# Performance work log

Measured on AMD Instinct MI355X. Metric: run time of the kernel, lower is better.

The kernel has to match this reference:

```python
import jax, jax.numpy as jnp
import numpy as np
import math

HEADS = 8
DIM_HEAD = 64
DIM = HEADS * DIM_HEAD  # 512; to_v is Identity so dim must equal heads*dim_head
SCALE = DIM_HEAD ** -0.5


def get_slopes(n):
    def pow2(n):
        start = 2 ** (-2 ** (-(math.log2(n) - 3)))
        return [start * start ** i for i in range(n)]
    if math.log2(n).is_integer():
        return pow2(n)
    c = 2 ** math.floor(math.log2(n))
    return pow2(c) + get_slopes(2 * c)[0::2][: n - c]

SLOPES = jnp.asarray(np.array(get_slopes(HEADS), dtype=np.float32))


def setup_inputs() -> dict:
    key = jax.random.key(0)
    k1, k2, k3, k4 = jax.random.split(key, 4)
    b, n = 4, 2048
    x = jax.random.normal(k1, (b, n, DIM), dtype=jnp.float32)
    # positions: e.g. observation timestamps (days); uniform floats scaled to [0, 365)
    positions = jax.random.uniform(k2, (b, n), dtype=jnp.float32) * 365.0
    Wq = jax.random.normal(k3, (DIM, DIM), dtype=jnp.float32) * (DIM ** -0.5)
    Wk = jax.random.normal(k4, (DIM, DIM), dtype=jnp.float32) * (DIM ** -0.5)
    return {"x": x, "positions": positions, "Wq": Wq, "Wk": Wk}


def reference(x, positions, Wq, Wk):
    b, n, _ = x.shape
    # q, k projections (no bias); v = x (Identity)
    q = (x @ Wq.T).reshape(b, n, HEADS, DIM_HEAD).transpose(0, 2, 1, 3)  # b h n d
    k = (x @ Wk.T).reshape(b, n, HEADS, DIM_HEAD).transpose(0, 2, 1, 3)
    v = x.reshape(b, n, HEADS, DIM_HEAD).transpose(0, 2, 1, 3)
    dots = jnp.einsum('bhid,bhjd->bhij', q, k) * SCALE  # b h n n
    # relative_positions[b,i,j] = -|positions[b,j] - positions[b,i]|
    rel = -jnp.abs(positions[:, None, :] - positions[:, :, None])  # b n n
    alibi = SLOPES[None, :, None, None] * rel[:, None, :, :]  # b h n n
    attn = jax.nn.softmax(dots + alibi, axis=-1)
    out = jnp.einsum('bhij,bhjd->bhid', attn, v)  # b h n d
    return out.transpose(0, 2, 1, 3).reshape(b, n, DIM)
```

## Files before the change

### kernel.cpp

```cpp
#include <hip/hip_runtime.h>
#include <hip/hip_bf16.h>

typedef __bf16 bf16x8 __attribute__((ext_vector_type(8)));
typedef float f32x4 __attribute__((ext_vector_type(4)));
typedef float f32x16 __attribute__((ext_vector_type(16)));

__device__ inline unsigned short f2bf(float f) {
    __hip_bfloat16 h = __float2bfloat16(f);
    return __builtin_bit_cast(unsigned short, h);
}
__device__ inline unsigned pk2bf(float a, float b) {
    return (unsigned)f2bf(a) | ((unsigned)f2bf(b) << 16);
}
__device__ inline float exp2_fast(float x) {
    float r;
    asm("v_exp_f32 %0, %1" : "=v"(r) : "v"(x));
    return r;
}

#define QSCALE 0.1803368801111244f

__global__ __launch_bounds__(256) void xpose_v(const float* __restrict__ x,
                                               unsigned short* __restrict__ Vt) {
    const int tid = threadIdx.x;
    const int lane = tid & 63, w = tid >> 6;
    const int b = blockIdx.z, h = blockIdx.y;
    const int n = blockIdx.x * 256 + w * 64 + lane;
    const int np = (n & ~15) | (n & 3) | ((n & 4) << 1) | ((n & 8) >> 1);
    const size_t xrow = ((size_t)b * 2048 + n) * 512 + h * 64;
    const size_t vbase = ((size_t)(b * 8 + h) * 64) * 2048 + np;
#pragma unroll
    for (int d0 = 0; d0 < 64; d0 += 4) {
        float4 v = *reinterpret_cast<const float4*>(&x[xrow + d0]);
        Vt[vbase + (size_t)(d0 + 0) * 2048] = f2bf(v.x);
        Vt[vbase + (size_t)(d0 + 1) * 2048] = f2bf(v.y);
        Vt[vbase + (size_t)(d0 + 2) * 2048] = f2bf(v.z);
        Vt[vbase + (size_t)(d0 + 3) * 2048] = f2bf(v.w);
    }
}

__global__ __launch_bounds__(256) void gemm_qk(const float* __restrict__ x,
                                               const float* __restrict__ Wq,
                                               const float* __restrict__ Wk,
                                               unsigned short* __restrict__ Qb,
                                               unsigned short* __restrict__ Kb) {
    __shared__ __align__(16) unsigned short sA[128 * 40];
    __shared__ __align__(16) unsigned short sB[128 * 40];
    const int tid  = threadIdx.x;
    const int lane = tid & 63;
    const int wave = tid >> 6;
    const int wr = wave >> 1, wc = wave & 1;
    const int bm = blockIdx.x * 128;
    const int by = blockIdx.y;
    const float* __restrict__ Bsrc = (by < 4) ? Wq : Wk;
    unsigned short* __restrict__ C = (by < 4) ? Qb : Kb;
    const int bn = (by & 3) * 128;
    const float scale = (by < 4) ? QSCALE : 1.0f;
    const int tr = tid >> 1, th = (tid & 1) * 16;
    const int rl = lane & 15;
    const int kq = (lane >> 4) * 8;

    f32x4 acc[4][4];
#pragma unroll
    for (int m = 0; m < 4; ++m)
#pragma unroll
        for (int n = 0; n < 4; ++n) acc[m][n] = (f32x4){0.f, 0.f, 0.f, 0.f};

    for (int k0 = 0; k0 < 512; k0 += 32) {
        const float* ap = &x[(size_t)(bm + tr) * 512 + k0 + th];
        const float* bp = &Bsrc[(size_t)(bn + tr) * 512 + k0 + th];
        float4 a0 = *reinterpret_cast<const float4*>(ap);
        float4 a1 = *reinterpret_cast<const float4*>(ap + 4);
        float4 a2 = *reinterpret_cast<const float4*>(ap + 8);
        float4 a3 = *reinterpret_cast<const float4*>(ap + 12);
        float4 b0 = *reinterpret_cast<const float4*>(bp);
        float4 b1 = *reinterpret_cast<const float4*>(bp + 4);
        float4 b2 = *reinterpret_cast<const float4*>(bp + 8);
        float4 b3 = *reinterpret_cast<const float4*>(bp + 12);
        uint4 pa0 = {pk2bf(a0.x, a0.y), pk2bf(a0.z, a0.w), pk2bf(a1.x, a1.y), pk2bf(a1.z, a1.w)};
        uint4 pa1 = {pk2bf(a2.x, a2.y), pk2bf(a2.z, a2.w), pk2bf(a3.x, a3.y), pk2bf(a3.z, a3.w)};
        uint4 pb0 = {pk2bf(b0.x, b0.y), pk2bf(b0.z, b0.w), pk2bf(b1.x, b1.y), pk2bf(b1.z, b1.w)};
        uint4 pb1 = {pk2bf(b2.x, b2.y), pk2bf(b2.z, b2.w), pk2bf(b3.x, b3.y), pk2bf(b3.z, b3.w)};
        __syncthreads();
        *reinterpret_cast<uint4*>(&sA[tr * 40 + th])     = pa0;
        *reinterpret_cast<uint4*>(&sA[tr * 40 + th + 8]) = pa1;
        *reinterpret_cast<uint4*>(&sB[tr * 40 + th])     = pb0;
        *reinterpret_cast<uint4*>(&sB[tr * 40 + th + 8]) = pb1;
        __syncthreads();

        bf16x8 af[4], bfv[4];
#pragma unroll
        for (int m = 0; m < 4; ++m)
            af[m] = __builtin_bit_cast(bf16x8,
                *reinterpret_cast<const uint4*>(&sA[(wr * 64 + m * 16 + rl) * 40 + kq]));
#pragma unroll
        for (int n = 0; n < 4; ++n)
            bfv[n] = __builtin_bit_cast(bf16x8,
                *reinterpret_cast<const uint4*>(&sB[(wc * 64 + n * 16 + rl) * 40 + kq]));
#pragma unroll
        for (int m = 0; m < 4; ++m)
#pragma unroll
            for (int n = 0; n < 4; ++n)
                acc[m][n] = __builtin_amdgcn_mfma_f32_16x16x32_bf16(af[m], bfv[n], acc[m][n], 0, 0, 0);
    }

    const int rq = (lane >> 4) * 4;
#pragma unroll
    for (int m = 0; m < 4; ++m) {
        int r = bm + wr * 64 + m * 16 + rq;
#pragma unroll
        for (int n = 0; n < 4; ++n) {
            int c = bn + wc * 64 + n * 16 + rl;
#pragma unroll
            for (int reg = 0; reg < 4; ++reg)
                C[(size_t)(r + reg) * 512 + c] = f2bf(acc[m][n][reg] * scale);
        }
    }
}

__global__ __launch_bounds__(512, 4) void attn_fwd(const unsigned short* __restrict__ Q,
                                                   const unsigned short* __restrict__ Kb,
                                                   const unsigned short* __restrict__ Vt,
                                                   const float* __restrict__ pos,
                                                   float* __restrict__ Out) {
    __shared__ __align__(16) unsigned char smem[34304];
    char* k0b = (char*)smem;
    char* v0b = (char*)smem + 8192;
    char* k1b = (char*)smem + 16384;
    char* v1b = (char*)smem + 24576;
    float* p0b = (float*)(smem + 32768);
    float* p1b = (float*)(smem + 33024);
    float* sMl = (float*)(smem + 33280);

    const int tid  = threadIdx.x;
    const int lane = tid & 63;
    const int w    = tid >> 6;
    const int l31  = lane & 31;
    const int hi   = lane >> 5;
    const int qh   = w & 3;
    const int jp   = w >> 2;
    const int b = blockIdx.z, h = blockIdx.y;
    const int q0 = blockIdx.x * 128 + qh * 32;
    const size_t rowbase = (size_t)b * 2048;
    const int hc = h * 64;
    const int bh = b * 8 + h;
    const float slopeL = ldexpf(1.4426950408889634f, -(h + 1));

    bf16x8 qf0, qf1, qf2, qf3;
    {
        const unsigned short* qp = &Q[(rowbase + q0 + l31) * 512 + hc + hi * 8];
        qf0 = __builtin_bit_cast(bf16x8, *reinterpret_cast<const uint4*>(qp));
        qf1 = __builtin_bit_cast(bf16x8, *reinterpret_cast<const uint4*>(qp + 16));
        qf2 = __builtin_bit_cast(bf16x8, *reinterpret_cast<const uint4*>(qp + 32));
        qf3 = __builtin_bit_cast(bf16x8, *reinterpret_cast<const uint4*>(qp + 48));
    }
    const float ui = slopeL * pos[rowbase + q0 + l31];

    float lloc = 0.f;
    f32x16 o0, o1;
#pragma unroll
    for (int r = 0; r < 16; ++r) { o0[r] = 0.f; o1[r] = 0.f; }

    const int sr  = tid >> 3;
    const int sce = (tid & 7) * 8;
    const int wbyte = sr * 128 + (((tid & 7) * 16) ^ ((sr & 7) << 4));
    const int kswz = (l31 & 7) << 4;

    uint4 ck, cv;
    float cpj = 0.f;

    auto stage = [&](int j0v) {
        ck = *reinterpret_cast<const uint4*>(&Kb[(rowbase + j0v + sr) * 512 + hc + sce]);
        cv = *reinterpret_cast<const uint4*>(&Vt[((size_t)bh * 64 + sr) * 2048 + j0v + sce]);
        if (tid < 64) cpj = pos[rowbase + j0v + tid];
    };
    auto writeb = [&](char* KB, char* VB, float* PB) {
        *reinterpret_cast<uint4*>(KB + wbyte) = ck;
        *reinterpret_cast<uint4*>(VB + wbyte) = cv;
        if (tid < 64) PB[tid] = slopeL * cpj;
    };
    auto compute = [&](const char* KB, const char* VB, const float* PB) {
        const char* kr = KB + (32 * jp + l31) * 128;
        f32x16 s;
#pragma unroll
        for (int r = 0; r < 16; ++r) s[r] = 0.f;
        __builtin_amdgcn_s_setprio(1);
#pragma unroll
        for (int ks = 0; ks < 4; ++ks) {
            bf16x8 kf = __builtin_bit_cast(bf16x8,
                *reinterpret_cast<const uint4*>(kr + ((ks * 32 + hi * 16) ^ kswz)));
            bf16x8 qq = (ks == 0) ? qf0 : (ks == 1) ? qf1 : (ks == 2) ? qf2 : qf3;
            s = __builtin_amdgcn_mfma_f32_32x32x16_bf16(kf, qq, s, 0, 0, 0);
        }
        __builtin_amdgcn_s_setprio(0);

        float ls = 0.f;
#pragma unroll
        for (int t = 0; t < 4; ++t) {
            f32x4 u = *reinterpret_cast<const f32x4*>(&PB[32 * jp + 8 * t + 4 * hi]);
#pragma unroll
            for (int r = 0; r < 4; ++r) {
                float p = exp2_fast(s[4 * t + r] - fabsf(u[r] - ui));
                s[4 * t + r] = p;
                ls += p;
            }
        }
        lloc += ls;

        bf16x8 pf0 = __builtin_bit_cast(bf16x8, (uint4){
            pk2bf(s[0], s[1]),  pk2bf(s[2], s[3]),   pk2bf(s[4], s[5]),   pk2bf(s[6], s[7])});
        bf16x8 pf1 = __builtin_bit_cast(bf16x8, (uint4){
            pk2bf(s[8], s[9]),  pk2bf(s[10], s[11]), pk2bf(s[12], s[13]), pk2bf(s[14], s[15])});

        const char* vr0 = VB + l31 * 128;
        const char* vr1 = VB + (32 + l31) * 128;
        __builtin_amdgcn_s_setprio(1);
#pragma unroll
        for (int ks = 0; ks < 2; ++ks) {
            const int cb = 64 * jp + ks * 32 + hi * 16;
            bf16x8 v0 = __builtin_bit_cast(bf16x8,
                *reinterpret_cast<const uint4*>(vr0 + (cb ^ kswz)));
            bf16x8 v1 = __builtin_bit_cast(bf16x8,
                *reinterpret_cast<const uint4*>(vr1 + (cb ^ kswz)));
            bf16x8 pf = ks ? pf1 : pf0;
            o0 = __builtin_amdgcn_mfma_f32_32x32x16_bf16(v0, pf, o0, 0, 0, 0);
            o1 = __builtin_amdgcn_mfma_f32_32x32x16_bf16(v1, pf, o1, 0, 0, 0);
        }
        __builtin_amdgcn_s_setprio(0);
    };

    stage(0);
    writeb(k0b, v0b, p0b);
    stage(64);
    __syncthreads();

    for (int t = 0; t < 32; t += 2) {
        writeb(k1b, v1b, p1b);
        if (t + 2 < 32) stage((t + 2) * 64);
        compute(k0b, v0b, p0b);
        __syncthreads();
        if (t + 2 < 32) {
            writeb(k0b, v0b, p0b);
            if (t + 3 < 32) stage((t + 3) * 64);
        }
        compute(k1b, v1b, p1b);
        __syncthreads();
    }

    float lt = lloc + __shfl_xor(lloc, 32, 64);
    float* sM = (float*)smem;
    const int key = (lane & 7) << 2;
    if (jp == 1) {
        float* dst = sM + qh * 2048 + lane * 32;
#pragma unroll
        for (int i = 0; i < 4; ++i) {
            f32x4 t0 = {o0[4 * i], o0[4 * i + 1], o0[4 * i + 2], o0[4 * i + 3]};
            f32x4 t1 = {o1[4 * i], o1[4 * i + 1], o1[4 * i + 2], o1[4 * i + 3]};
            *reinterpret_cast<f32x4*>(dst + ((4 * i) ^ key))      = t0;
            *reinterpret_cast<f32x4*>(dst + ((16 + 4 * i) ^ key)) = t1;
        }
        sMl[qh * 64 + lane] = lt;
    }
    __syncthreads();
    if (jp == 0) {
        const float* src = sM + qh * 2048 + lane * 32;
#pragma unroll
        for (int i = 0; i < 4; ++i) {
            f32x4 t0 = *reinterpret_cast<const f32x4*>(src + ((4 * i) ^ key));
            f32x4 t1 = *reinterpret_cast<const f32x4*>(src + ((16 + 4 * i) ^ key));
#pragma unroll
            for (int r = 0; r < 4; ++r) { o0[4 * i + r] += t0[r]; o1[4 * i + r] += t1[r]; }
        }
        const float linv = 1.0f / (lt + sMl[qh * 64 + lane]);
        float* orow = &Out[(rowbase + q0 + l31) * 512 + hc];
#pragma unroll
        for (int t = 0; t < 4; ++t) {
            f32x4 a, c;
#pragma unroll
            for (int r = 0; r < 4; ++r) {
                a[r] = o0[4 * t + r] * linv;
                c[r] = o1[4 * t + r] * linv;
            }
            *reinterpret_cast<f32x4*>(orow + 8 * t + 4 * hi)      = a;
            *reinterpret_cast<f32x4*>(orow + 32 + 8 * t + 4 * hi) = c;
        }
    }
}

extern "C" void kernel_launch(void* const* d_in, const int* in_sizes, int n_in,
                              void* d_out, int out_size, void* d_ws, size_t ws_size,
                              hipStream_t stream) {
    const float* x   = (const float*)d_in[0];
    const float* pos = (const float*)d_in[1];
    const float* Wq  = (const float*)d_in[2];
    const float* Wk  = (const float*)d_in[3];
    float* out = (float*)d_out;

    unsigned short* Qb  = (unsigned short*)d_ws;
    unsigned short* Kbf = Qb  + 4194304;
    unsigned short* Vtb = Kbf + 4194304;

    xpose_v<<<dim3(8, 8, 4), dim3(256), 0, stream>>>(x, Vtb);
    gemm_qk<<<dim3(64, 8), dim3(256), 0, stream>>>(x, Wq, Wk, Qb, Kbf);
    attn_fwd<<<dim3(16, 8, 4), dim3(512), 0, stream>>>(Qb, Kbf, Vtb, pos, out);
}
```

Baseline: 86.47 us.

## Double KV tile to 128 keys per iteration and use packed bf16 convert

Each iteration of the attention loop now processes 128 keys instead of 64, so each wave handles two 32-key score blocks. This halves the number of loop iterations and block-wide barriers, and gives more independent MFMAs to overlap with the exp and softmax work. Converting probabilities to bf16 now uses the v_cvt_pk_bf16_f32 instruction instead of scalar conversions. In exchange, shared memory roughly doubles to about 66KB and register use rises, which may cut occupancy below the 4 blocks requested in the launch bounds.

```diff
diff --git a/kernel.cpp b/kernel.cpp
--- a/kernel.cpp
+++ b/kernel.cpp
@@ -11,6 +11,11 @@
 }
 __device__ inline unsigned pk2bf(float a, float b) {
     return (unsigned)f2bf(a) | ((unsigned)f2bf(b) << 16);
+}
+__device__ inline unsigned cvtpk(float a, float b) {
+    unsigned r;
+    asm("v_cvt_pk_bf16_f32 %0, %1, %2" : "=v"(r) : "v"(a), "v"(b));
+    return r;
 }
 __device__ inline float exp2_fast(float x) {
     float r;
@@ -123,14 +128,14 @@
                                                    const unsigned short* __restrict__ Vt,
                                                    const float* __restrict__ pos,
                                                    float* __restrict__ Out) {
-    __shared__ __align__(16) unsigned char smem[34304];
+    __shared__ __align__(16) unsigned char smem[67584];
     char* k0b = (char*)smem;
-    char* v0b = (char*)smem + 8192;
-    char* k1b = (char*)smem + 16384;
-    char* v1b = (char*)smem + 24576;
-    float* p0b = (float*)(smem + 32768);
-    float* p1b = (float*)(smem + 33024);
-    float* sMl = (float*)(smem + 33280);
+    char* v0b = (char*)smem + 16384;
+    char* k1b = (char*)smem + 32768;
+    char* v1b = (char*)smem + 49152;
+    float* p0b = (float*)(smem + 65536);
+    float* p1b = (float*)(smem + 66048);
+    float* sMl = (float*)(smem + 66560);
 
     const int tid  = threadIdx.x;
     const int lane = tid & 63;
@@ -161,68 +166,85 @@
 #pragma unroll
     for (int r = 0; r < 16; ++r) { o0[r] = 0.f; o1[r] = 0.f; }
 
-    const int sr  = tid >> 3;
-    const int sce = (tid & 7) * 8;
-    const int wbyte = sr * 128 + (((tid & 7) * 16) ^ ((sr & 7) << 4));
+    const int srk = tid >> 2, sck = (tid & 3) * 16;
+    const int wkb0 = srk * 128 + (((tid & 3) * 32) ^ ((srk & 7) << 4));
+    const int wkb1 = srk * 128 + ((((tid & 3) * 32) + 16) ^ ((srk & 7) << 4));
+    const int srv = tid >> 3, scv = (tid & 7) * 16;
+    const int wvb0 = srv * 256 + (((tid & 7) * 32) ^ ((srv & 7) << 4));
+    const int wvb1 = srv * 256 + ((((tid & 7) * 32) + 16) ^ ((srv & 7) << 4));
     const int kswz = (l31 & 7) << 4;
 
-    uint4 ck, cv;
+    uint4 ck0, ck1, cv0, cv1;
     float cpj = 0.f;
 
     auto stage = [&](int j0v) {
-        ck = *reinterpret_cast<const uint4*>(&Kb[(rowbase + j0v + sr) * 512 + hc + sce]);
-        cv = *reinterpret_cast<const uint4*>(&Vt[((size_t)bh * 64 + sr) * 2048 + j0v + sce]);
-        if (tid < 64) cpj = pos[rowbase + j0v + tid];
+        const unsigned short* kp = &Kb[(rowbase + j0v + srk) * 512 + hc + sck];
+        const unsigned short* vp = &Vt[((size_t)bh * 64 + srv) * 2048 + j0v + scv];
+        ck0 = *reinterpret_cast<const uint4*>(kp);
+        ck1 = *reinterpret_cast<const uint4*>(kp + 8);
+        cv0 = *reinterpret_cast<const uint4*>(vp);
+        cv1 = *reinterpret_cast<const uint4*>(vp + 8);
+        if (tid < 128) cpj = pos[rowbase + j0v + tid];
     };
     auto writeb = [&](char* KB, char* VB, float* PB) {
-        *reinterpret_cast<uint4*>(KB + wbyte) = ck;
-        *reinterpret_cast<uint4*>(VB + wbyte) = cv;
-        if (tid < 64) PB[tid] = slopeL * cpj;
+        *reinterpret_cast<uint4*>(KB + wkb0) = ck0;
+        *reinterpret_cast<uint4*>(KB + wkb1) = ck1;
+        *reinterpret_cast<uint4*>(VB + wvb0) = cv0;
+        *reinterpret_cast<uint4*>(VB + wvb1) = cv1;
+        if (tid < 128) PB[tid] = slopeL * cpj;
     };
     auto compute = [&](const char* KB, const char* VB, const float* PB) {
-        const char* kr = KB + (32 * jp + l31) * 128;
-        f32x16 s;
-#pragma unroll
-        for (int r = 0; r < 16; ++r) s[r] = 0.f;
+        const char* kr0 = KB + (64 * jp + l31) * 128;
+        const char* kr1 = kr0 + 32 * 128;
+        f32x16 s0, s1;
+#pragma unroll
+        for (int r = 0; r < 16; ++r) { s0[r] = 0.f; s1[r] = 0.f; }
         __builtin_amdgcn_s_setprio(1);
 #pragma unroll
         for (int ks = 0; ks < 4; ++ks) {
-            bf16x8 kf = __builtin_bit_cast(bf16x8,
-                *reinterpret_cast<const uint4*>(kr + ((ks * 32 + hi * 16) ^ kswz)));
+            const int off = (ks * 32 + hi * 16) ^ kswz;
+            bf16x8 kf0 = __builtin_bit_cast(bf16x8, *reinterpret_cast<const uint4*>(kr0 + off));
+            bf16x8 kf1 = __builtin_bit_cast(bf16x8, *reinterpret_cast<const uint4*>(kr1 + off));
             bf16x8 qq = (ks == 0) ? qf0 : (ks == 1) ? qf1 : (ks == 2) ? qf2 : qf3;
-            s = __builtin_amdgcn_mfma_f32_32x32x16_bf16(kf, qq, s, 0, 0, 0);
+            s0 = __builtin_amdgcn_mfma_f32_32x32x16_bf16(kf0, qq, s0, 0, 0, 0);
+            s1 = __builtin_amdgcn_mfma_f32_32x32x16_bf16(kf1, qq, s1, 0, 0, 0);
         }
         __builtin_amdgcn_s_setprio(0);
 
         float ls = 0.f;
 #pragma unroll
         for (int t = 0; t < 4; ++t) {
-            f32x4 u = *reinterpret_cast<const f32x4*>(&PB[32 * jp + 8 * t + 4 * hi]);
+            f32x4 u0 = *reinterpret_cast<const f32x4*>(&PB[64 * jp + 8 * t + 4 * hi]);
+            f32x4 u1 = *reinterpret_cast<const f32x4*>(&PB[64 * jp + 32 + 8 * t + 4 * hi]);
 #pragma unroll
             for (int r = 0; r < 4; ++r) {
-                float p = exp2_fast(s[4 * t + r] - fabsf(u[r] - ui));
-                s[4 * t + r] = p;
-                ls += p;
+                float p0 = exp2_fast(s0[4 * t + r] - fabsf(u0[r] - ui));
+                float p1 = exp2_fast(s1[4 * t + r] - fabsf(u1[r] - ui));
+                s0[4 * t + r] = p0;
+                s1[4 * t + r] = p1;
+                ls += p0 + p1;
             }
         }
         lloc += ls;
 
         bf16x8 pf0 = __builtin_bit_cast(bf16x8, (uint4){
-            pk2bf(s[0], s[1]),  pk2bf(s[2], s[3]),   pk2bf(s[4], s[5]),   pk2bf(s[6], s[7])});
+            cvtpk(s0[0], s0[1]),  cvtpk(s0[2], s0[3]),   cvtpk(s0[4], s0[5]),   cvtpk(s0[6], s0[7])});
         bf16x8 pf1 = __builtin_bit_cast(bf16x8, (uint4){
-            pk2bf(s[8], s[9]),  pk2bf(s[10], s[11]), pk2bf(s[12], s[13]), pk2bf(s[14], s[15])});
-
-        const char* vr0 = VB + l31 * 128;
-        const char* vr1 = VB + (32 + l31) * 128;
+            cvtpk(s0[8], s0[9]),  cvtpk(s0[10], s0[11]), cvtpk(s0[12], s0[13]), cvtpk(s0[14], s0[15])});
+        bf16x8 pf2 = __builtin_bit_cast(bf16x8, (uint4){
+            cvtpk(s1[0], s1[1]),  cvtpk(s1[2], s1[3]),   cvtpk(s1[4], s1[5]),   cvtpk(s1[6], s1[7])});
+        bf16x8 pf3 = __builtin_bit_cast(bf16x8, (uint4){
+            cvtpk(s1[8], s1[9]),  cvtpk(s1[10], s1[11]), cvtpk(s1[12], s1[13]), cvtpk(s1[14], s1[15])});
+
+        const char* vr0 = VB + l31 * 256;
+        const char* vr1 = VB + (32 + l31) * 256;
         __builtin_amdgcn_s_setprio(1);
 #pragma unroll
-        for (int ks = 0; ks < 2; ++ks) {
-            const int cb = 64 * jp + ks * 32 + hi * 16;
-            bf16x8 v0 = __builtin_bit_cast(bf16x8,
-                *reinterpret_cast<const uint4*>(vr0 + (cb ^ kswz)));
-            bf16x8 v1 = __builtin_bit_cast(bf16x8,
-                *reinterpret_cast<const uint4*>(vr1 + (cb ^ kswz)));
-            bf16x8 pf = ks ? pf1 : pf0;
+        for (int ks = 0; ks < 4; ++ks) {
+            const int cb = (jp * 128 + ks * 32 + hi * 16) ^ kswz;
+            bf16x8 v0 = __builtin_bit_cast(bf16x8, *reinterpret_cast<const uint4*>(vr0 + cb));
+            bf16x8 v1 = __builtin_bit_cast(bf16x8, *reinterpret_cast<const uint4*>(vr1 + cb));
+            bf16x8 pf = (ks == 0) ? pf0 : (ks == 1) ? pf1 : (ks == 2) ? pf2 : pf3;
             o0 = __builtin_amdgcn_mfma_f32_32x32x16_bf16(v0, pf, o0, 0, 0, 0);
             o1 = __builtin_amdgcn_mfma_f32_32x32x16_bf16(v1, pf, o1, 0, 0, 0);
         }
@@ -231,17 +253,17 @@
 
     stage(0);
     writeb(k0b, v0b, p0b);
-    stage(64);
+    stage(128);
     __syncthreads();
 
-    for (int t = 0; t < 32; t += 2) {
+    for (int t = 0; t < 16; t += 2) {
         writeb(k1b, v1b, p1b);
-        if (t + 2 < 32) stage((t + 2) * 64);
+        if (t + 2 < 16) stage((t + 2) * 128);
         compute(k0b, v0b, p0b);
         __syncthreads();
-        if (t + 2 < 32) {
+        if (t + 2 < 16) {
             writeb(k0b, v0b, p0b);
-            if (t + 3 < 32) stage((t + 3) * 64);
+            if (t + 3 < 16) stage((t + 3) * 128);
         }
         compute(k1b, v1b, p1b);
         __syncthreads();
```

New measurement: 129.2 us. 1.49x slower.

## Compute softmax row sums via MFMA with ones and remap blocks for XCD locality

Applied to the files above, without the earlier changes.

The per-element scalar accumulation of softmax denominators is replaced by an extra MFMA that multiplies a ones matrix by the bf16 probability fragment, so the row sum comes out of the matrix unit. This removes VALU adds and the final cross-lane shuffle, but it adds MFMA work and sums the bf16-rounded probabilities rather than the fp32 values. Separately, the 3D grid becomes a flat 1D grid remapped so that consecutive blocks on the same XCD (flat & 7) share a batch-head. The aim is better L2 reuse of K and V per chiplet.

```diff
diff --git a/kernel.cpp b/kernel.cpp
--- a/kernel.cpp
+++ b/kernel.cpp
@@ -139,11 +139,15 @@
     const int hi   = lane >> 5;
     const int qh   = w & 3;
     const int jp   = w >> 2;
-    const int b = blockIdx.z, h = blockIdx.y;
-    const int q0 = blockIdx.x * 128 + qh * 32;
+    const int flat = blockIdx.x;
+    const int xcd  = flat & 7;
+    const int idx  = flat >> 3;
+    const int bh   = xcd * 4 + (idx >> 4);
+    const int qt   = idx & 15;
+    const int b = bh >> 3, h = bh & 7;
+    const int q0 = qt * 128 + qh * 32;
     const size_t rowbase = (size_t)b * 2048;
     const int hc = h * 64;
-    const int bh = b * 8 + h;
     const float slopeL = ldexpf(1.4426950408889634f, -(h + 1));
 
     bf16x8 qf0, qf1, qf2, qf3;
@@ -155,11 +159,12 @@
         qf3 = __builtin_bit_cast(bf16x8, *reinterpret_cast<const uint4*>(qp + 48));
     }
     const float ui = slopeL * pos[rowbase + q0 + l31];
-
-    float lloc = 0.f;
-    f32x16 o0, o1;
-#pragma unroll
-    for (int r = 0; r < 16; ++r) { o0[r] = 0.f; o1[r] = 0.f; }
+    const bf16x8 ones = __builtin_bit_cast(bf16x8,
+        (uint4){0x3F803F80u, 0x3F803F80u, 0x3F803F80u, 0x3F803F80u});
+
+    f32x16 o0, o1, lacc;
+#pragma unroll
+    for (int r = 0; r < 16; ++r) { o0[r] = 0.f; o1[r] = 0.f; lacc[r] = 0.f; }
 
     const int sr  = tid >> 3;
     const int sce = (tid & 7) * 8;
@@ -194,18 +199,13 @@
         }
         __builtin_amdgcn_s_setprio(0);
 
-        float ls = 0.f;
 #pragma unroll
         for (int t = 0; t < 4; ++t) {
             f32x4 u = *reinterpret_cast<const f32x4*>(&PB[32 * jp + 8 * t + 4 * hi]);
 #pragma unroll
-            for (int r = 0; r < 4; ++r) {
-                float p = exp2_fast(s[4 * t + r] - fabsf(u[r] - ui));
-                s[4 * t + r] = p;
-                ls += p;
-            }
-        }
-        lloc += ls;
+            for (int r = 0; r < 4; ++r)
+                s[4 * t + r] = exp2_fast(s[4 * t + r] - fabsf(u[r] - ui));
+        }
 
         bf16x8 pf0 = __builtin_bit_cast(bf16x8, (uint4){
             pk2bf(s[0], s[1]),  pk2bf(s[2], s[3]),   pk2bf(s[4], s[5]),   pk2bf(s[6], s[7])});
@@ -217,14 +217,13 @@
         __builtin_amdgcn_s_setprio(1);
 #pragma unroll
         for (int ks = 0; ks < 2; ++ks) {
-            const int cb = 64 * jp + ks * 32 + hi * 16;
-            bf16x8 v0 = __builtin_bit_cast(bf16x8,
-                *reinterpret_cast<const uint4*>(vr0 + (cb ^ kswz)));
-            bf16x8 v1 = __builtin_bit_cast(bf16x8,
-                *reinterpret_cast<const uint4*>(vr1 + (cb ^ kswz)));
+            const int cb = (64 * jp + ks * 32 + hi * 16) ^ kswz;
+            bf16x8 v0 = __builtin_bit_cast(bf16x8, *reinterpret_cast<const uint4*>(vr0 + cb));
+            bf16x8 v1 = __builtin_bit_cast(bf16x8, *reinterpret_cast<const uint4*>(vr1 + cb));
             bf16x8 pf = ks ? pf1 : pf0;
             o0 = __builtin_amdgcn_mfma_f32_32x32x16_bf16(v0, pf, o0, 0, 0, 0);
             o1 = __builtin_amdgcn_mfma_f32_32x32x16_bf16(v1, pf, o1, 0, 0, 0);
+            lacc = __builtin_amdgcn_mfma_f32_32x32x16_bf16(ones, pf, lacc, 0, 0, 0);
         }
         __builtin_amdgcn_s_setprio(0);
     };
@@ -247,7 +246,7 @@
         __syncthreads();
     }
 
-    float lt = lloc + __shfl_xor(lloc, 32, 64);
+    const float lt = lacc[0];
     float* sM = (float*)smem;
     const int key = (lane & 7) << 2;
     if (jp == 1) {
@@ -302,5 +301,5 @@
 
     xpose_v<<<dim3(8, 8, 4), dim3(256), 0, stream>>>(x, Vtb);
     gemm_qk<<<dim3(64, 8), dim3(256), 0, stream>>>(x, Wq, Wk, Qb, Kbf);
-    attn_fwd<<<dim3(16, 8, 4), dim3(512), 0, stream>>>(Qb, Kbf, Vtb, pos, out);
-}
+    attn_fwd<<<dim3(512), dim3(512), 0, stream>>>(Qb, Kbf, Vtb, pos, out);
+}
```

New measurement: 92.90 us. +7.4%, slower.

## Load K/V fragments directly from global memory, shrink blocks, remap grid per XCD

Applied to the files above, without the earlier changes.

The attention kernel stops staging K and V tiles through double-buffered shared memory. Each wave now loads its MFMA fragments straight from global memory (relying on L2 reuse), with register prefetch of the next K tile, and the per-tile barriers go away. Blocks shrink to 256 threads covering 64 query rows. A flat 1024-block grid maps each group of batch-heads to one XCD for L2 locality, and all positions for the batch are pre-scaled once into shared memory. The cost is more global and L2 traffic because K/V are loaded per wave rather than shared across waves, and more register use for the prefetched fragments.

```diff
diff --git a/kernel.cpp b/kernel.cpp
--- a/kernel.cpp
+++ b/kernel.cpp
@@ -118,32 +118,30 @@
     }
 }
 
-__global__ __launch_bounds__(512, 4) void attn_fwd(const unsigned short* __restrict__ Q,
+__global__ __launch_bounds__(256, 4) void attn_fwd(const unsigned short* __restrict__ Q,
                                                    const unsigned short* __restrict__ Kb,
                                                    const unsigned short* __restrict__ Vt,
                                                    const float* __restrict__ pos,
                                                    float* __restrict__ Out) {
-    __shared__ __align__(16) unsigned char smem[34304];
-    char* k0b = (char*)smem;
-    char* v0b = (char*)smem + 8192;
-    char* k1b = (char*)smem + 16384;
-    char* v1b = (char*)smem + 24576;
-    float* p0b = (float*)(smem + 32768);
-    float* p1b = (float*)(smem + 33024);
-    float* sMl = (float*)(smem + 33280);
+    __shared__ __align__(16) unsigned char smem[16896];
+    float* sPos = (float*)smem;
 
     const int tid  = threadIdx.x;
     const int lane = tid & 63;
     const int w    = tid >> 6;
     const int l31  = lane & 31;
     const int hi   = lane >> 5;
-    const int qh   = w & 3;
-    const int jp   = w >> 2;
-    const int b = blockIdx.z, h = blockIdx.y;
-    const int q0 = blockIdx.x * 128 + qh * 32;
+    const int qh   = w & 1;
+    const int jp   = w >> 1;
+    const int flat = blockIdx.x;
+    const int xcd  = flat & 7;
+    const int idx  = flat >> 3;
+    const int bh   = xcd * 4 + (idx >> 5);
+    const int qt   = idx & 31;
+    const int b = bh >> 3, h = bh & 7;
+    const int q0 = qt * 64 + qh * 32;
     const size_t rowbase = (size_t)b * 2048;
     const int hc = h * 64;
-    const int bh = b * 8 + h;
     const float slopeL = ldexpf(1.4426950408889634f, -(h + 1));
 
     bf16x8 qf0, qf1, qf2, qf3;
@@ -156,52 +154,61 @@
     }
     const float ui = slopeL * pos[rowbase + q0 + l31];
 
+    {
+        f32x4* sp4 = (f32x4*)sPos;
+        const float4* gp4 = (const float4*)(pos + rowbase);
+#pragma unroll
+        for (int i = 0; i < 2; ++i) {
+            float4 v = gp4[tid + 256 * i];
+            sp4[tid + 256 * i] = (f32x4){v.x * slopeL, v.y * slopeL, v.z * slopeL, v.w * slopeL};
+        }
+    }
+    __syncthreads();
+
     float lloc = 0.f;
     f32x16 o0, o1;
 #pragma unroll
     for (int r = 0; r < 16; ++r) { o0[r] = 0.f; o1[r] = 0.f; }
 
-    const int sr  = tid >> 3;
-    const int sce = (tid & 7) * 8;
-    const int wbyte = sr * 128 + (((tid & 7) * 16) ^ ((sr & 7) << 4));
-    const int kswz = (l31 & 7) << 4;
-
-    uint4 ck, cv;
-    float cpj = 0.f;
-
-    auto stage = [&](int j0v) {
-        ck = *reinterpret_cast<const uint4*>(&Kb[(rowbase + j0v + sr) * 512 + hc + sce]);
-        cv = *reinterpret_cast<const uint4*>(&Vt[((size_t)bh * 64 + sr) * 2048 + j0v + sce]);
-        if (tid < 64) cpj = pos[rowbase + j0v + tid];
+    const unsigned short* Kbase  = &Kb[(rowbase + 32 * jp + l31) * 512 + hc + hi * 8];
+    const unsigned short* Vbase0 = &Vt[((size_t)bh * 64 + l31) * 2048 + 32 * jp + 8 * hi];
+    const unsigned short* Vbase1 = Vbase0 + (size_t)32 * 2048;
+
+    auto loadK = [&](int t, uint4& k0, uint4& k1, uint4& k2, uint4& k3) {
+        const unsigned short* kp = Kbase + (size_t)t * 64 * 512;
+        k0 = *reinterpret_cast<const uint4*>(kp);
+        k1 = *reinterpret_cast<const uint4*>(kp + 16);
+        k2 = *reinterpret_cast<const uint4*>(kp + 32);
+        k3 = *reinterpret_cast<const uint4*>(kp + 48);
     };
-    auto writeb = [&](char* KB, char* VB, float* PB) {
-        *reinterpret_cast<uint4*>(KB + wbyte) = ck;
-        *reinterpret_cast<uint4*>(VB + wbyte) = cv;
-        if (tid < 64) PB[tid] = slopeL * cpj;
-    };
-    auto compute = [&](const char* KB, const char* VB, const float* PB) {
-        const char* kr = KB + (32 * jp + l31) * 128;
+
+    auto tile = [&](int t, uint4 k0, uint4 k1, uint4 k2, uint4 k3) {
+        const int j0 = 64 * t + 32 * jp;
+        const unsigned short* vp0 = Vbase0 + t * 64;
+        const unsigned short* vp1 = Vbase1 + t * 64;
+        uint4 v00 = *reinterpret_cast<const uint4*>(vp0);
+        uint4 v01 = *reinterpret_cast<const uint4*>(vp0 + 16);
+        uint4 v10 = *reinterpret_cast<const uint4*>(vp1);
+        uint4 v11 = *reinterpret_cast<const uint4*>(vp1 + 16);
+
         f32x16 s;
 #pragma unroll
         for (int r = 0; r < 16; ++r) s[r] = 0.f;
         __builtin_amdgcn_s_setprio(1);
-#pragma unroll
-        for (int ks = 0; ks < 4; ++ks) {
-            bf16x8 kf = __builtin_bit_cast(bf16x8,
-                *reinterpret_cast<const uint4*>(kr + ((ks * 32 + hi * 16) ^ kswz)));
-            bf16x8 qq = (ks == 0) ? qf0 : (ks == 1) ? qf1 : (ks == 2) ? qf2 : qf3;
-            s = __builtin_amdgcn_mfma_f32_32x32x16_bf16(kf, qq, s, 0, 0, 0);
-        }
+        s = __builtin_amdgcn_mfma_f32_32x32x16_bf16(__builtin_bit_cast(bf16x8, k0), qf0, s, 0, 0, 0);
+        s = __builtin_amdgcn_mfma_f32_32x32x16_bf16(__builtin_bit_cast(bf16x8, k1), qf1, s, 0, 0, 0);
+        s = __builtin_amdgcn_mfma_f32_32x32x16_bf16(__builtin_bit_cast(bf16x8, k2), qf2, s, 0, 0, 0);
+        s = __builtin_amdgcn_mfma_f32_32x32x16_bf16(__builtin_bit_cast(bf16x8, k3), qf3, s, 0, 0, 0);
         __builtin_amdgcn_s_setprio(0);
 
         float ls = 0.f;
 #pragma unroll
-        for (int t = 0; t < 4; ++t) {
-            f32x4 u = *reinterpret_cast<const f32x4*>(&PB[32 * jp + 8 * t + 4 * hi]);
+        for (int tt = 0; tt < 4; ++tt) {
+            f32x4 u = *reinterpret_cast<const f32x4*>(&sPos[j0 + 8 * tt + 4 * hi]);
 #pragma unroll
             for (int r = 0; r < 4; ++r) {
-                float p = exp2_fast(s[4 * t + r] - fabsf(u[r] - ui));
-                s[4 * t + r] = p;
+                float p = exp2_fast(s[4 * tt + r] - fabsf(u[r] - ui));
+                s[4 * tt + r] = p;
                 ls += p;
             }
         }
@@ -212,46 +219,30 @@
         bf16x8 pf1 = __builtin_bit_cast(bf16x8, (uint4){
             pk2bf(s[8], s[9]),  pk2bf(s[10], s[11]), pk2bf(s[12], s[13]), pk2bf(s[14], s[15])});
 
-        const char* vr0 = VB + l31 * 128;
-        const char* vr1 = VB + (32 + l31) * 128;
         __builtin_amdgcn_s_setprio(1);
-#pragma unroll
-        for (int ks = 0; ks < 2; ++ks) {
-            const int cb = 64 * jp + ks * 32 + hi * 16;
-            bf16x8 v0 = __builtin_bit_cast(bf16x8,
-                *reinterpret_cast<const uint4*>(vr0 + (cb ^ kswz)));
-            bf16x8 v1 = __builtin_bit_cast(bf16x8,
-                *reinterpret_cast<const uint4*>(vr1 + (cb ^ kswz)));
-            bf16x8 pf = ks ? pf1 : pf0;
-            o0 = __builtin_amdgcn_mfma_f32_32x32x16_bf16(v0, pf, o0, 0, 0, 0);
-            o1 = __builtin_amdgcn_mfma_f32_32x32x16_bf16(v1, pf, o1, 0, 0, 0);
-        }
+        o0 = __builtin_amdgcn_mfma_f32_32x32x16_bf16(__builtin_bit_cast(bf16x8, v00), pf0, o0, 0, 0, 0);
+        o1 = __builtin_amdgcn_mfma_f32_32x32x16_bf16(__builtin_bit_cast(bf16x8, v10), pf0, o1, 0, 0, 0);
+        o0 = __builtin_amdgcn_mfma_f32_32x32x16_bf16(__builtin_bit_cast(bf16x8, v01), pf1, o0, 0, 0, 0);
+        o1 = __builtin_amdgcn_mfma_f32_32x32x16_bf16(__builtin_bit_cast(bf16x8, v11), pf1, o1, 0, 0, 0);
         __builtin_amdgcn_s_setprio(0);
     };
 
-    stage(0);
-    writeb(k0b, v0b, p0b);
-    stage(64);
+    uint4 a0, a1, a2, a3, c0, c1, c2, c3;
+    loadK(0, a0, a1, a2, a3);
+    for (int t = 0; t < 32; t += 2) {
+        if (t + 1 < 32) loadK(t + 1, c0, c1, c2, c3);
+        tile(t, a0, a1, a2, a3);
+        if (t + 2 < 32) loadK(t + 2, a0, a1, a2, a3);
+        if (t + 1 < 32) tile(t + 1, c0, c1, c2, c3);
+    }
+
+    float lt = lloc + __shfl_xor(lloc, 32, 64);
     __syncthreads();
-
-    for (int t = 0; t < 32; t += 2) {
-        writeb(k1b, v1b, p1b);
-        if (t + 2 < 32) stage((t + 2) * 64);
-        compute(k0b, v0b, p0b);
-        __syncthreads();
-        if (t + 2 < 32) {
-            writeb(k0b, v0b, p0b);
-            if (t + 3 < 32) stage((t + 3) * 64);
-        }
-        compute(k1b, v1b, p1b);
-        __syncthreads();
-    }
-
-    float lt = lloc + __shfl_xor(lloc, 32, 64);
-    float* sM = (float*)smem;
+    float* sMf = (float*)smem;
+    float* sMl = sMf + 4096;
     const int key = (lane & 7) << 2;
     if (jp == 1) {
-        float* dst = sM + qh * 2048 + lane * 32;
+        float* dst = sMf + qh * 2048 + lane * 32;
 #pragma unroll
         for (int i = 0; i < 4; ++i) {
             f32x4 t0 = {o0[4 * i], o0[4 * i + 1], o0[4 * i + 2], o0[4 * i + 3]};
@@ -263,7 +254,7 @@
     }
     __syncthreads();
     if (jp == 0) {
-        const float* src = sM + qh * 2048 + lane * 32;
+        const float* src = sMf + qh * 2048 + lane * 32;
 #pragma unroll
         for (int i = 0; i < 4; ++i) {
             f32x4 t0 = *reinterpret_cast<const f32x4*>(src + ((4 * i) ^ key));
@@ -302,5 +293,5 @@
 
     xpose_v<<<dim3(8, 8, 4), dim3(256), 0, stream>>>(x, Vtb);
     gemm_qk<<<dim3(64, 8), dim3(256), 0, stream>>>(x, Wq, Wk, Qb, Kbf);
-    attn_fwd<<<dim3(16, 8, 4), dim3(512), 0, stream>>>(Qb, Kbf, Vtb, pos, out);
-}
+    attn_fwd<<<dim3(1024), dim3(256), 0, stream>>>(Qb, Kbf, Vtb, pos, out);
+}
```

Result: slower. 184.0 us (+112.8%).
